# Kernel optimization log

Measured on AMD Instinct MI355X. Metric: run time of the kernel, lower is better.

## Reference

```python
import jax, jax.numpy as jnp
import numpy as np

B, H, I = 64, 1024, 512
MIN_TAU = 1e-3  # max(1e-5, config.CELL_MIN_TAU=0.001)


def setup_inputs() -> dict:
    key = jax.random.key(0)
    k1, k2, k3, k4, k5 = jax.random.split(key, 5)
    x_t = jax.random.normal(k1, (B, I), dtype=jnp.float32)
    h_prev = jax.random.normal(k2, (B, H), dtype=jnp.float32)
    # Linear init scale ~ 1/sqrt(fan_in); xavier for W_hh
    W_ih = jax.random.normal(k3, (H, I), dtype=jnp.float32) * (1.0 / np.sqrt(I))
    b_ih = jnp.zeros((H,), dtype=jnp.float32)
    W_hh = jax.random.normal(k4, (H, H), dtype=jnp.float32) * np.sqrt(2.0 / (H + H))
    temperature = jnp.asarray(1.0, dtype=jnp.float32)
    # Gumbel(0,1) noise, fixed at setup for determinism: g = -log(-log(U))
    u = jax.random.uniform(k5, (B, H, H), dtype=jnp.float32, minval=1e-8, maxval=1.0 - 1e-8)
    gumbel_noise = -jnp.log(-jnp.log(u))
    return {"x_t": x_t, "h_prev": h_prev, "W_ih": W_ih, "b_ih": b_ih,
            "W_hh": W_hh, "temperature": temperature, "gumbel_noise": gumbel_noise}


def reference(x_t, h_prev, W_ih, b_ih, W_hh, temperature, gumbel_noise):
    # ReservoirRNNCell.forward (eval mode, soft sampling, hh_mask == ones)
    tau = jnp.maximum(temperature, MIN_TAU)
    input_contrib = x_t @ W_ih.T + b_ih                      # (B, H)
    logits = (W_hh / tau)[None, :, :] + gumbel_noise          # (B, H, H)
    y = jax.nn.softmax(logits, axis=2)                        # gumbel_softmax(tau=1, hard=False)
    contrib = jnp.einsum('boh,bh->bo', y, h_prev)             # routed hidden mix
    h_next = jnp.tanh(input_contrib + contrib)                # (B, H)
    return h_next
```

## Files before the change

kernel.cpp:

```cpp
#include <hip/hip_runtime.h>
#include <hip/hip_bf16.h>
#include <math.h>


constexpr int B_ = 64;
constexpr int H_ = 1024;
constexpr int I_ = 512;

__global__ __launch_bounds__(256) void reservoir_fused_kernel(
    const float* __restrict__ x_t,
    const float* __restrict__ h_prev,
    const float* __restrict__ W_ih,
    const float* __restrict__ b_ih,
    const float* __restrict__ W_hh,
    const float* __restrict__ temperature,
    const float* __restrict__ gumbel,
    float* __restrict__ out)
{
    const int gtid = blockIdx.x * blockDim.x + threadIdx.x;
    const int wave = gtid >> 6;
    const int lane = gtid & 63;
    const int b = wave >> 10;
    const int o = wave & (H_ - 1);

    const float tau = fmaxf(temperature[0], 1e-3f);
    const float inv_tau = 1.0f / tau;

    float ic = 0.0f;
    {
        const float4* x4 = reinterpret_cast<const float4*>(x_t + (size_t)b * I_);
        const float4* w4 = reinterpret_cast<const float4*>(W_ih + (size_t)o * I_);
#pragma unroll
        for (int c = 0; c < I_ / 256; ++c) {
            float4 xv = x4[c * 64 + lane];
            float4 wv = w4[c * 64 + lane];
            ic = fmaf(xv.x, wv.x, ic);
            ic = fmaf(xv.y, wv.y, ic);
            ic = fmaf(xv.z, wv.z, ic);
            ic = fmaf(xv.w, wv.w, ic);
        }
    }

    float s = 0.0f, t = 0.0f;
    {
        const float4* g4 = reinterpret_cast<const float4*>(gumbel + ((size_t)b * H_ + o) * H_);
        const float4* w4 = reinterpret_cast<const float4*>(W_hh + (size_t)o * H_);
        const float4* h4 = reinterpret_cast<const float4*>(h_prev + (size_t)b * H_);
#pragma unroll
        for (int c = 0; c < 4; ++c) {
            float4 g = g4[c * 64 + lane];
            float4 w = w4[c * 64 + lane];
            float4 h = h4[c * 64 + lane];
            float e0 = __expf(fmaf(w.x, inv_tau, g.x));
            float e1 = __expf(fmaf(w.y, inv_tau, g.y));
            float e2 = __expf(fmaf(w.z, inv_tau, g.z));
            float e3 = __expf(fmaf(w.w, inv_tau, g.w));
            s += (e0 + e1) + (e2 + e3);
            t = fmaf(e0, h.x, t);
            t = fmaf(e1, h.y, t);
            t = fmaf(e2, h.z, t);
            t = fmaf(e3, h.w, t);
        }
    }

#pragma unroll
    for (int off = 32; off > 0; off >>= 1) {
        s  += __shfl_xor(s,  off, 64);
        t  += __shfl_xor(t,  off, 64);
        ic += __shfl_xor(ic, off, 64);
    }

    if (lane == 0) {
        float res = tanhf(ic + b_ih[o] + t / s);
        out[(size_t)b * H_ + o] = res;
    }
}

extern "C" void kernel_launch(void* const* d_in, const int* in_sizes, int n_in,
                              void* d_out, int out_size, void* d_ws, size_t ws_size,
                              hipStream_t stream) {
    const float* x_t    = (const float*)d_in[0];
    const float* h_prev = (const float*)d_in[1];
    const float* W_ih   = (const float*)d_in[2];
    const float* b_ih   = (const float*)d_in[3];
    const float* W_hh   = (const float*)d_in[4];
    const float* temp   = (const float*)d_in[5];
    const float* gum    = (const float*)d_in[6];
    float* out = (float*)d_out;

    const int total_waves = B_ * H_;
    const int blocks = total_waves / 4;
    reservoir_fused_kernel<<<blocks, 256, 0, stream>>>(
        x_t, h_prev, W_ih, b_ih, W_hh, temp, gum, out);
}
```

Baseline: 362.9 us.

## Map four output rows per wave using 16-lane groups

Work is remapped so each 64-lane wave handles four (b,o) rows with 16 lanes per row instead of one row per wave. Each lane now loops over more elements with split accumulators, and the shuffle reduction shrinks to 16-lane width. The goal is to cut reduction and launch overhead per row and give each lane more memory-level parallelism on the gumbel stream. In exchange each lane carries longer serial loops with more registers, and there are four times fewer blocks.

```diff
diff --git a/kernel.cpp b/kernel.cpp
--- a/kernel.cpp
+++ b/kernel.cpp
@@ -18,22 +18,23 @@
     float* __restrict__ out)
 {
     const int gtid = blockIdx.x * blockDim.x + threadIdx.x;
-    const int wave = gtid >> 6;
-    const int lane = gtid & 63;
-    const int b = wave >> 10;
-    const int o = wave & (H_ - 1);
+    const int lane = threadIdx.x & 63;
+    const int q    = lane >> 4;
+    const int ql   = lane & 15;
+    const int row  = (gtid >> 6) * 4 + q;
+    const int b = row >> 10;
+    const int o = row & (H_ - 1);
 
-    const float tau = fmaxf(temperature[0], 1e-3f);
-    const float inv_tau = 1.0f / tau;
+    const float inv_tau = 1.0f / fmaxf(temperature[0], 1e-3f);
 
     float ic = 0.0f;
     {
         const float4* x4 = reinterpret_cast<const float4*>(x_t + (size_t)b * I_);
         const float4* w4 = reinterpret_cast<const float4*>(W_ih + (size_t)o * I_);
 #pragma unroll
-        for (int c = 0; c < I_ / 256; ++c) {
-            float4 xv = x4[c * 64 + lane];
-            float4 wv = w4[c * 64 + lane];
+        for (int c = 0; c < 8; ++c) {
+            float4 xv = x4[c * 16 + ql];
+            float4 wv = w4[c * 16 + ql];
             ic = fmaf(xv.x, wv.x, ic);
             ic = fmaf(xv.y, wv.y, ic);
             ic = fmaf(xv.z, wv.z, ic);
@@ -41,38 +42,40 @@
         }
     }
 
-    float s = 0.0f, t = 0.0f;
+    float s0 = 0.f, s1 = 0.f, t0 = 0.f, t1 = 0.f;
     {
-        const float4* g4 = reinterpret_cast<const float4*>(gumbel + ((size_t)b * H_ + o) * H_);
+        const float4* g4 = reinterpret_cast<const float4*>(gumbel) + (size_t)row * (H_ / 4);
         const float4* w4 = reinterpret_cast<const float4*>(W_hh + (size_t)o * H_);
         const float4* h4 = reinterpret_cast<const float4*>(h_prev + (size_t)b * H_);
-#pragma unroll
-        for (int c = 0; c < 4; ++c) {
-            float4 g = g4[c * 64 + lane];
-            float4 w = w4[c * 64 + lane];
-            float4 h = h4[c * 64 + lane];
+#pragma unroll 4
+        for (int c = 0; c < 16; ++c) {
+            float4 g = g4[c * 16 + ql];
+            float4 w = w4[c * 16 + ql];
+            float4 h = h4[c * 16 + ql];
             float e0 = __expf(fmaf(w.x, inv_tau, g.x));
             float e1 = __expf(fmaf(w.y, inv_tau, g.y));
             float e2 = __expf(fmaf(w.z, inv_tau, g.z));
             float e3 = __expf(fmaf(w.w, inv_tau, g.w));
-            s += (e0 + e1) + (e2 + e3);
-            t = fmaf(e0, h.x, t);
-            t = fmaf(e1, h.y, t);
-            t = fmaf(e2, h.z, t);
-            t = fmaf(e3, h.w, t);
+            s0 += e0 + e1;
+            s1 += e2 + e3;
+            t0 = fmaf(e0, h.x, t0);
+            t1 = fmaf(e1, h.y, t1);
+            t0 = fmaf(e2, h.z, t0);
+            t1 = fmaf(e3, h.w, t1);
         }
     }
+    float s = s0 + s1;
+    float t = t0 + t1;
 
 #pragma unroll
-    for (int off = 32; off > 0; off >>= 1) {
-        s  += __shfl_xor(s,  off, 64);
-        t  += __shfl_xor(t,  off, 64);
-        ic += __shfl_xor(ic, off, 64);
+    for (int off = 8; off > 0; off >>= 1) {
+        s  += __shfl_xor(s,  off, 16);
+        t  += __shfl_xor(t,  off, 16);
+        ic += __shfl_xor(ic, off, 16);
     }
 
-    if (lane == 0) {
-        float res = tanhf(ic + b_ih[o] + t / s);
-        out[(size_t)b * H_ + o] = res;
+    if (ql == 0) {
+        out[row] = tanhf(ic + b_ih[o] + t / s);
     }
 }
 
@@ -88,8 +91,7 @@
     const float* gum    = (const float*)d_in[6];
     float* out = (float*)d_out;
 
-    const int total_waves = B_ * H_;
-    const int blocks = total_waves / 4;
+    const int blocks = (B_ * H_) / 16;
     reservoir_fused_kernel<<<blocks, 256, 0, stream>>>(
         x_t, h_prev, W_ih, b_ih, W_hh, temp, gum, out);
 }
```

Result: slower. 401.9 us (+10.8%).
